# Optimization experiments

Measured on AMD Instinct MI355X. Metric: run time of the kernel, lower is better.

Reference implementation:

```python
import jax, jax.numpy as jnp
import numpy as np

N = 50000
E = 1600000
F_IN = 128
F_OUT = 64
NEG_SLOPE = 0.2


def setup_inputs() -> dict:
    key = jax.random.key(0)
    k1, k2, k3, k4, k5, k6 = jax.random.split(key, 6)
    x = jax.random.normal(k1, (N, F_IN), dtype=jnp.float32)
    edge_index = jax.random.randint(k2, (2, E), 0, N, dtype=jnp.int64)
    # GATConv params (heads=1): glorot-ish scale
    W = jax.random.normal(k3, (F_IN, F_OUT), dtype=jnp.float32) * (1.0 / np.sqrt(F_IN))
    att_src = jax.random.normal(k4, (F_OUT,), dtype=jnp.float32) * (1.0 / np.sqrt(F_OUT))
    att_dst = jax.random.normal(k5, (F_OUT,), dtype=jnp.float32) * (1.0 / np.sqrt(F_OUT))
    bias = jnp.zeros((F_OUT,), dtype=jnp.float32)
    return {"x": x, "edge_index": edge_index, "W": W, "att_src": att_src, "att_dst": att_dst, "bias": bias}


def _gat_forward(x, edge_index, W, att_src, att_dst, bias):
    n = x.shape[0]
    # add self loops (PyG GATConv default)
    loops = jnp.arange(n, dtype=edge_index.dtype)
    src = jnp.concatenate([edge_index[0], loops])  # [E+N]
    dst = jnp.concatenate([edge_index[1], loops])  # [E+N]

    h = x @ W                                      # [N, F_OUT]
    a_src = h @ att_src                            # [N]
    a_dst = h @ att_dst                            # [N]

    e = a_src[src] + a_dst[dst]                    # [E+N]
    e = jnp.where(e > 0, e, NEG_SLOPE * e)         # LeakyReLU(0.2)

    # softmax over edges grouped by destination node
    e_max = jax.ops.segment_max(e, dst, num_segments=n)     # [N]
    e_exp = jnp.exp(e - e_max[dst])                          # [E+N]
    e_sum = jax.ops.segment_sum(e_exp, dst, num_segments=n)  # [N]
    alpha = e_exp / e_sum[dst]                               # [E+N]

    msg = h[src] * alpha[:, None]                            # [E+N, F_OUT]
    out = jax.ops.segment_sum(msg, dst, num_segments=n)      # [N, F_OUT]
    out = out + bias
    return jax.nn.relu(out)


def reference(x, edge_index, W, att_src, att_dst, bias):
    return _gat_forward(x, edge_index, W, att_src, att_dst, bias)
```

## Files before the change

kernel.cpp:

```cpp
#include <hip/hip_runtime.h>

#define NN 50000
#define NE 1600000
#define FIN 128
#define FOUT 64
#define SLOPE 0.2f

#define NBC  63
#define NPC  800
#define CAPC 27500
#define NPB  16
#define NFPB 50
#define NBF  (NBC * NFPB)
#define CAPB 768
#define FBLK 261
#define CHC4 1536
#define GBLK 782
#define K2PB 8
#define LW   136

typedef unsigned int u32;
typedef short short8 __attribute__((ext_vector_type(8)));
typedef float f32x4 __attribute__((ext_vector_type(4)));

__device__ __forceinline__ unsigned short f2bf(float f) {
    u32 u = __float_as_uint(f);
    u += 0x7FFFu + ((u >> 16) & 1u);
    return (unsigned short)(u >> 16);
}
__device__ __forceinline__ float bf2f(unsigned short s) {
    return __uint_as_float(((u32)s) << 16);
}

union FusedLds {
    unsigned short Wt[64 * LW];
    struct { int cnt[4][64]; int gb[64]; int cur[64]; } f;
};

__global__ __launch_bounds__(256) void fused_k(
        const float* __restrict__ x, const float* __restrict__ W,
        const float* __restrict__ att_s, const float* __restrict__ att_d,
        const int* __restrict__ ei, int* __restrict__ ccur,
        u32* __restrict__ cstage, unsigned short* __restrict__ h,
        float* __restrict__ a_src, float* __restrict__ a_dst) {
    __shared__ FusedLds L;
    const int tid = threadIdx.x;

    if (blockIdx.x < FBLK) {
        const int wv = tid >> 6;
        ((int*)L.f.cnt)[tid] = 0;
        __syncthreads();
        const int4* sd4 = (const int4*)(ei + NE);
        const int4* ss4 = (const int4*)ei;
        const int lo = blockIdx.x * CHC4, hi = min(NE / 4, lo + CHC4);
        for (int i = lo + tid; i < hi; i += 256) {
            int4 d = sd4[i];
            atomicAdd(&L.f.cnt[wv][d.x / NPC], 1);
            atomicAdd(&L.f.cnt[wv][d.y / NPC], 1);
            atomicAdd(&L.f.cnt[wv][d.z / NPC], 1);
            atomicAdd(&L.f.cnt[wv][d.w / NPC], 1);
        }
        __syncthreads();
        if (tid < NBC) {
            int tot = L.f.cnt[0][tid] + L.f.cnt[1][tid]
                    + L.f.cnt[2][tid] + L.f.cnt[3][tid];
            L.f.gb[tid] = tot ? atomicAdd(&ccur[tid], tot) : 0;
            L.f.cur[tid] = 0;
        }
        __syncthreads();
        for (int i = lo + tid; i < hi; i += 256) {
            int4 d = sd4[i];
            int4 s = ss4[i];
            int b, pos;
            b = d.x / NPC; pos = L.f.gb[b] + atomicAdd(&L.f.cur[b], 1);
            if (pos < CAPC) cstage[b * CAPC + pos] = (u32)s.x | ((u32)(d.x - b * NPC) << 16);
            b = d.y / NPC; pos = L.f.gb[b] + atomicAdd(&L.f.cur[b], 1);
            if (pos < CAPC) cstage[b * CAPC + pos] = (u32)s.y | ((u32)(d.y - b * NPC) << 16);
            b = d.z / NPC; pos = L.f.gb[b] + atomicAdd(&L.f.cur[b], 1);
            if (pos < CAPC) cstage[b * CAPC + pos] = (u32)s.z | ((u32)(d.z - b * NPC) << 16);
            b = d.w / NPC; pos = L.f.gb[b] + atomicAdd(&L.f.cur[b], 1);
            if (pos < CAPC) cstage[b * CAPC + pos] = (u32)s.w | ((u32)(d.w - b * NPC) << 16);
        }
    } else {
        unsigned short* Wt = L.Wt;
        const int node0 = (blockIdx.x - FBLK) * 64;
        for (int i = tid; i < 128 * 16; i += 256) {
            int k = i >> 4, f = (i & 15) * 4;
            float4 w4 = ((const float4*)W)[i];
            Wt[(f + 0) * LW + k] = f2bf(w4.x);
            Wt[(f + 1) * LW + k] = f2bf(w4.y);
            Wt[(f + 2) * LW + k] = f2bf(w4.z);
            Wt[(f + 3) * LW + k] = f2bf(w4.w);
        }
        const int wv = tid >> 6, lane = tid & 63;
        const int q = lane >> 4, mr = lane & 15;
        const int row = node0 + wv * 16 + mr;
        const bool valid = row < NN;
        const float4* x4 = (const float4*)x;

        short8 afr[4];
        #pragma unroll
        for (int ks = 0; ks < 4; ++ks) {
            float4 f0 = make_float4(0.f, 0.f, 0.f, 0.f), f1 = f0;
            if (valid) {
                f0 = x4[(size_t)row * 32 + ks * 8 + q * 2];
                f1 = x4[(size_t)row * 32 + ks * 8 + q * 2 + 1];
            }
            short8 a;
            a[0] = (short)f2bf(f0.x); a[1] = (short)f2bf(f0.y);
            a[2] = (short)f2bf(f0.z); a[3] = (short)f2bf(f0.w);
            a[4] = (short)f2bf(f1.x); a[5] = (short)f2bf(f1.y);
            a[6] = (short)f2bf(f1.z); a[7] = (short)f2bf(f1.w);
            afr[ks] = a;
        }
        __syncthreads();

        f32x4 acc[4] = {{0,0,0,0},{0,0,0,0},{0,0,0,0},{0,0,0,0}};
        #pragma unroll
        for (int ks = 0; ks < 4; ++ks) {
            #pragma unroll
            for (int nt = 0; nt < 4; ++nt) {
                short8 b = *(const short8*)(Wt + (nt * 16 + mr) * LW + ks * 32 + q * 8);
                acc[nt] = __builtin_amdgcn_mfma_f32_16x16x32_bf16(afr[ks], b, acc[nt], 0, 0, 0);
            }
        }
        float atts[4], attd[4];
        #pragma unroll
        for (int nt = 0; nt < 4; ++nt) {
            atts[nt] = att_s[nt * 16 + mr];
            attd[nt] = att_d[nt * 16 + mr];
        }
        #pragma unroll
        for (int r = 0; r < 4; ++r) {
            int node = node0 + wv * 16 + q * 4 + r;
            float ps = 0.f, pd = 0.f;
            #pragma unroll
            for (int nt = 0; nt < 4; ++nt) {
                float v = acc[nt][r];
                if (node < NN) h[(size_t)node * 64 + nt * 16 + mr] = f2bf(v);
                ps += v * atts[nt];
                pd += v * attd[nt];
            }
            #pragma unroll
            for (int off = 8; off > 0; off >>= 1) {
                ps += __shfl_xor(ps, off);
                pd += __shfl_xor(pd, off);
            }
            if (mr == 0 && node < NN) { a_src[node] = ps; a_dst[node] = pd; }
        }
    }
}

__global__ __launch_bounds__(256) void fine_k(
        const u32* __restrict__ cstage, const int* __restrict__ ccur,
        int* __restrict__ fcur, u32* __restrict__ fstage) {
    const int bin = blockIdx.x / K2PB, sub = blockIdx.x % K2PB;
    const int size = min(ccur[bin], CAPC);
    const int qs = (size + K2PB - 1) / K2PB;
    const int lo = sub * qs, hi = min(size, lo + qs);
    const u32* src = cstage + (size_t)bin * CAPC;
    const int tid = threadIdx.x, wv = tid >> 6;

    __shared__ int cnt[4][64];
    __shared__ int gb[64];
    __shared__ int cur[64];
    ((int*)cnt)[tid] = 0;
    __syncthreads();
    for (int i = lo + tid; i < hi; i += 256)
        atomicAdd(&cnt[wv][(src[i] >> 16) >> 4], 1);
    __syncthreads();
    if (tid < NFPB) {
        int tot = cnt[0][tid] + cnt[1][tid] + cnt[2][tid] + cnt[3][tid];
        gb[tid] = tot ? atomicAdd(&fcur[bin * NFPB + tid], tot) : 0;
        cur[tid] = 0;
    }
    __syncthreads();
    for (int i = lo + tid; i < hi; i += 256) {
        u32 w = src[i];
        int dl = w >> 16;
        int f = dl >> 4;
        int pos = gb[f] + atomicAdd(&cur[f], 1);
        if (pos < CAPB)
            fstage[(size_t)(bin * NFPB + f) * CAPB + pos] =
                (w & 0xFFFFu) | ((u32)(dl & 15) << 16);
    }
}

__global__ __launch_bounds__(256) void agg_k(
        const u32* __restrict__ staging, const int* __restrict__ bcur,
        const float* __restrict__ a_src, const float* __restrict__ a_dst,
        const ushort4* __restrict__ h4, const float* __restrict__ bias,
        float* __restrict__ out) {
    const int bkt = blockIdx.x;
    const int node0 = bkt << 4;
    if (node0 >= NN) return;
    const int nNodes = min(NPB, NN - node0);
    const int bsize = min(bcur[bkt], CAPB);
    const u32* stg = staging + (size_t)bkt * CAPB;
    const int tid = threadIdx.x, wv = tid >> 6, lane = tid & 63;

    __shared__ u32 pk[CAPB];
    __shared__ unsigned short ssrc[CAPB];
    __shared__ int lcnt[NPB];
    __shared__ int lbase[NPB + 1];
    __shared__ int lcur[NPB];
    float* evals = (float*)pk;

    for (int j = tid; j < bsize; j += 256) pk[j] = stg[j];
    if (tid < NPB) lcnt[tid] = 0;
    __syncthreads();
    for (int j = tid; j < bsize; j += 256)
        atomicAdd(&lcnt[pk[j] >> 16], 1);
    __syncthreads();
    if (tid < 64) {
        int v = (tid < NPB) ? lcnt[tid] : 0;
        #pragma unroll
        for (int off = 1; off < NPB; off <<= 1) {
            int u = __shfl_up(v, off);
            if (tid >= off) v += u;
        }
        if (tid < NPB) lbase[tid + 1] = v;
        if (tid == 0) lbase[0] = 0;
    }
    if (tid >= 64 && tid < 64 + NPB) lcur[tid - 64] = 0;
    __syncthreads();
    for (int j = tid; j < bsize; j += 256) {
        u32 w = pk[j];
        int ld = w >> 16;
        int pos = lbase[ld] + atomicAdd(&lcur[ld], 1);
        ssrc[pos] = (unsigned short)(w & 0xFFFFu);
    }
    __syncthreads();

    const int q = lane >> 4, ql = lane & 15;
    const float4 b4 = ((const float4*)bias)[ql];
    const int ln = wv * 4 + q;
    if (ln >= nNodes) return;
    const int n = node0 + ln;
    const int st = lbase[ln], deg = lbase[ln + 1] - st;
    const float ad = a_dst[n];
    float es = a_src[n] + ad; es = es > 0.f ? es : SLOPE * es;
    const float ps = __expf(es);
    float sum = 0.f;
    for (int j = ql; j < deg; j += 16) {
        int s = ssrc[st + j];
        float e = a_src[s] + ad; e = e > 0.f ? e : SLOPE * e;
        float pe = __expf(e);
        evals[st + j] = pe;
        sum += pe;
    }
    sum += __shfl_xor(sum, 8); sum += __shfl_xor(sum, 4);
    sum += __shfl_xor(sum, 2); sum += __shfl_xor(sum, 1);
    const float inv = 1.f / (sum + ps);

    ushort4 hs = h4[(size_t)n * 16 + ql];
    float a0 = ps * bf2f(hs.x), a1 = ps * bf2f(hs.y);
    float a2 = ps * bf2f(hs.z), a3 = ps * bf2f(hs.w);
    int j = 0;
    for (; j + 4 <= deg; j += 4) {
        int s0 = ssrc[st + j], s1 = ssrc[st + j + 1];
        int s2 = ssrc[st + j + 2], s3 = ssrc[st + j + 3];
        float e0 = evals[st + j], e1 = evals[st + j + 1];
        float e2 = evals[st + j + 2], e3 = evals[st + j + 3];
        ushort4 v0 = h4[(size_t)s0 * 16 + ql];
        ushort4 v1 = h4[(size_t)s1 * 16 + ql];
        ushort4 v2 = h4[(size_t)s2 * 16 + ql];
        ushort4 v3 = h4[(size_t)s3 * 16 + ql];
        a0 += e0 * bf2f(v0.x); a1 += e0 * bf2f(v0.y);
        a2 += e0 * bf2f(v0.z); a3 += e0 * bf2f(v0.w);
        a0 += e1 * bf2f(v1.x); a1 += e1 * bf2f(v1.y);
        a2 += e1 * bf2f(v1.z); a3 += e1 * bf2f(v1.w);
        a0 += e2 * bf2f(v2.x); a1 += e2 * bf2f(v2.y);
        a2 += e2 * bf2f(v2.z); a3 += e2 * bf2f(v2.w);
        a0 += e3 * bf2f(v3.x); a1 += e3 * bf2f(v3.y);
        a2 += e3 * bf2f(v3.z); a3 += e3 * bf2f(v3.w);
    }
    for (; j < deg; ++j) {
        int s = ssrc[st + j];
        float ev = evals[st + j];
        ushort4 hv = h4[(size_t)s * 16 + ql];
        a0 += ev * bf2f(hv.x); a1 += ev * bf2f(hv.y);
        a2 += ev * bf2f(hv.z); a3 += ev * bf2f(hv.w);
    }
    float4 o;
    o.x = a0 * inv + b4.x; o.x = o.x > 0.f ? o.x : 0.f;
    o.y = a1 * inv + b4.y; o.y = o.y > 0.f ? o.y : 0.f;
    o.z = a2 * inv + b4.z; o.z = o.z > 0.f ? o.z : 0.f;
    o.w = a3 * inv + b4.w; o.w = o.w > 0.f ? o.w : 0.f;
    ((float4*)out)[(size_t)n * 16 + ql] = o;
}

extern "C" void kernel_launch(void* const* d_in, const int* in_sizes, int n_in,
                              void* d_out, int out_size, void* d_ws, size_t ws_size,
                              hipStream_t stream) {
    const float* x     = (const float*)d_in[0];
    const int*   ei    = (const int*)d_in[1];
    const float* W     = (const float*)d_in[2];
    const float* att_s = (const float*)d_in[3];
    const float* att_d = (const float*)d_in[4];
    const float* bias  = (const float*)d_in[5];
    float* out = (float*)d_out;

    unsigned short* h = (unsigned short*)d_ws;
    float* a_src  = (float*)(h + (size_t)NN * 64);
    float* a_dst  = a_src + NN;
    int*   ccur   = (int*)(a_dst + NN);
    int*   fcur   = ccur + 64;
    u32*   cstage = (u32*)(fcur + 3200);
    u32*   fstage = cstage + (size_t)NBC * CAPC;

    hipMemsetAsync(ccur, 0, (64 + 3200) * sizeof(int), stream);

    fused_k<<<FBLK + GBLK, 256, 0, stream>>>(x, W, att_s, att_d, ei, ccur,
                                             cstage, h, a_src, a_dst);
    fine_k<<<NBC * K2PB, 256, 0, stream>>>(cstage, ccur, fcur, fstage);
    agg_k<<<NBF, 256, 0, stream>>>(fstage, fcur, a_src, a_dst,
                                   (const ushort4*)h, bias, out);
}
```

Baseline: 143.4 us.

## Replace two-level edge binning with single-pass 64-node buckets

Drops the coarse/fine two-pass radix binning: the fused kernel now scatters edges directly into 782 buckets of 64 destination nodes each, and the separate fine_k kernel is removed. The aggregation kernel handles 64 nodes per block, with each 16-lane quad looping over 4 nodes. This saves one kernel launch and a full read/write pass over the staged edges. The cost is more global atomics per block (up to 782 bins), LDS counters spread across many bins, and fewer, larger aggregation blocks with serialized per-quad work.

```diff
diff --git a/kernel.cpp b/kernel.cpp
--- a/kernel.cpp
+++ b/kernel.cpp
@@ -6,17 +6,12 @@
 #define FOUT 64
 #define SLOPE 0.2f
 
-#define NBC  63
-#define NPC  800
-#define CAPC 27500
-#define NPB  16
-#define NFPB 50
-#define NBF  (NBC * NFPB)
-#define CAPB 768
+#define NPB  64
+#define NB   782
+#define CAP  2560
 #define FBLK 261
 #define CHC4 1536
 #define GBLK 782
-#define K2PB 8
 #define LW   136
 
 typedef unsigned int u32;
@@ -34,7 +29,7 @@
 
 union FusedLds {
     unsigned short Wt[64 * LW];
-    struct { int cnt[4][64]; int gb[64]; int cur[64]; } f;
+    struct { int cnt[NB]; int gb[NB]; int cur[NB]; } f;
 };
 
 __global__ __launch_bounds__(256) void fused_k(
@@ -47,39 +42,37 @@
     const int tid = threadIdx.x;
 
     if (blockIdx.x < FBLK) {
-        const int wv = tid >> 6;
-        ((int*)L.f.cnt)[tid] = 0;
+        for (int i = tid; i < NB; i += 256) L.f.cnt[i] = 0;
         __syncthreads();
         const int4* sd4 = (const int4*)(ei + NE);
         const int4* ss4 = (const int4*)ei;
         const int lo = blockIdx.x * CHC4, hi = min(NE / 4, lo + CHC4);
         for (int i = lo + tid; i < hi; i += 256) {
             int4 d = sd4[i];
-            atomicAdd(&L.f.cnt[wv][d.x / NPC], 1);
-            atomicAdd(&L.f.cnt[wv][d.y / NPC], 1);
-            atomicAdd(&L.f.cnt[wv][d.z / NPC], 1);
-            atomicAdd(&L.f.cnt[wv][d.w / NPC], 1);
-        }
-        __syncthreads();
-        if (tid < NBC) {
-            int tot = L.f.cnt[0][tid] + L.f.cnt[1][tid]
-                    + L.f.cnt[2][tid] + L.f.cnt[3][tid];
-            L.f.gb[tid] = tot ? atomicAdd(&ccur[tid], tot) : 0;
-            L.f.cur[tid] = 0;
+            atomicAdd(&L.f.cnt[d.x >> 6], 1);
+            atomicAdd(&L.f.cnt[d.y >> 6], 1);
+            atomicAdd(&L.f.cnt[d.z >> 6], 1);
+            atomicAdd(&L.f.cnt[d.w >> 6], 1);
+        }
+        __syncthreads();
+        for (int b = tid; b < NB; b += 256) {
+            int tot = L.f.cnt[b];
+            L.f.gb[b] = tot ? atomicAdd(&ccur[b], tot) : 0;
+            L.f.cur[b] = 0;
         }
         __syncthreads();
         for (int i = lo + tid; i < hi; i += 256) {
             int4 d = sd4[i];
             int4 s = ss4[i];
             int b, pos;
-            b = d.x / NPC; pos = L.f.gb[b] + atomicAdd(&L.f.cur[b], 1);
-            if (pos < CAPC) cstage[b * CAPC + pos] = (u32)s.x | ((u32)(d.x - b * NPC) << 16);
-            b = d.y / NPC; pos = L.f.gb[b] + atomicAdd(&L.f.cur[b], 1);
-            if (pos < CAPC) cstage[b * CAPC + pos] = (u32)s.y | ((u32)(d.y - b * NPC) << 16);
-            b = d.z / NPC; pos = L.f.gb[b] + atomicAdd(&L.f.cur[b], 1);
-            if (pos < CAPC) cstage[b * CAPC + pos] = (u32)s.z | ((u32)(d.z - b * NPC) << 16);
-            b = d.w / NPC; pos = L.f.gb[b] + atomicAdd(&L.f.cur[b], 1);
-            if (pos < CAPC) cstage[b * CAPC + pos] = (u32)s.w | ((u32)(d.w - b * NPC) << 16);
+            b = d.x >> 6; pos = L.f.gb[b] + atomicAdd(&L.f.cur[b], 1);
+            if (pos < CAP) cstage[(size_t)b * CAP + pos] = (u32)s.x | ((u32)(d.x & 63) << 16);
+            b = d.y >> 6; pos = L.f.gb[b] + atomicAdd(&L.f.cur[b], 1);
+            if (pos < CAP) cstage[(size_t)b * CAP + pos] = (u32)s.y | ((u32)(d.y & 63) << 16);
+            b = d.z >> 6; pos = L.f.gb[b] + atomicAdd(&L.f.cur[b], 1);
+            if (pos < CAP) cstage[(size_t)b * CAP + pos] = (u32)s.z | ((u32)(d.z & 63) << 16);
+            b = d.w >> 6; pos = L.f.gb[b] + atomicAdd(&L.f.cur[b], 1);
+            if (pos < CAP) cstage[(size_t)b * CAP + pos] = (u32)s.w | ((u32)(d.w & 63) << 16);
         }
     } else {
         unsigned short* Wt = L.Wt;
@@ -151,56 +144,20 @@
     }
 }
 
-__global__ __launch_bounds__(256) void fine_k(
-        const u32* __restrict__ cstage, const int* __restrict__ ccur,
-        int* __restrict__ fcur, u32* __restrict__ fstage) {
-    const int bin = blockIdx.x / K2PB, sub = blockIdx.x % K2PB;
-    const int size = min(ccur[bin], CAPC);
-    const int qs = (size + K2PB - 1) / K2PB;
-    const int lo = sub * qs, hi = min(size, lo + qs);
-    const u32* src = cstage + (size_t)bin * CAPC;
-    const int tid = threadIdx.x, wv = tid >> 6;
-
-    __shared__ int cnt[4][64];
-    __shared__ int gb[64];
-    __shared__ int cur[64];
-    ((int*)cnt)[tid] = 0;
-    __syncthreads();
-    for (int i = lo + tid; i < hi; i += 256)
-        atomicAdd(&cnt[wv][(src[i] >> 16) >> 4], 1);
-    __syncthreads();
-    if (tid < NFPB) {
-        int tot = cnt[0][tid] + cnt[1][tid] + cnt[2][tid] + cnt[3][tid];
-        gb[tid] = tot ? atomicAdd(&fcur[bin * NFPB + tid], tot) : 0;
-        cur[tid] = 0;
-    }
-    __syncthreads();
-    for (int i = lo + tid; i < hi; i += 256) {
-        u32 w = src[i];
-        int dl = w >> 16;
-        int f = dl >> 4;
-        int pos = gb[f] + atomicAdd(&cur[f], 1);
-        if (pos < CAPB)
-            fstage[(size_t)(bin * NFPB + f) * CAPB + pos] =
-                (w & 0xFFFFu) | ((u32)(dl & 15) << 16);
-    }
-}
-
 __global__ __launch_bounds__(256) void agg_k(
         const u32* __restrict__ staging, const int* __restrict__ bcur,
         const float* __restrict__ a_src, const float* __restrict__ a_dst,
         const ushort4* __restrict__ h4, const float* __restrict__ bias,
         float* __restrict__ out) {
     const int bkt = blockIdx.x;
-    const int node0 = bkt << 4;
-    if (node0 >= NN) return;
+    const int node0 = bkt << 6;
     const int nNodes = min(NPB, NN - node0);
-    const int bsize = min(bcur[bkt], CAPB);
-    const u32* stg = staging + (size_t)bkt * CAPB;
+    const int bsize = min(bcur[bkt], CAP);
+    const u32* stg = staging + (size_t)bkt * CAP;
     const int tid = threadIdx.x, wv = tid >> 6, lane = tid & 63;
 
-    __shared__ u32 pk[CAPB];
-    __shared__ unsigned short ssrc[CAPB];
+    __shared__ u32 pk[CAP];
+    __shared__ unsigned short ssrc[CAP];
     __shared__ int lcnt[NPB];
     __shared__ int lbase[NPB + 1];
     __shared__ int lcur[NPB];
@@ -213,13 +170,13 @@
         atomicAdd(&lcnt[pk[j] >> 16], 1);
     __syncthreads();
     if (tid < 64) {
-        int v = (tid < NPB) ? lcnt[tid] : 0;
-        #pragma unroll
-        for (int off = 1; off < NPB; off <<= 1) {
+        int v = lcnt[tid];
+        #pragma unroll
+        for (int off = 1; off < 64; off <<= 1) {
             int u = __shfl_up(v, off);
             if (tid >= off) v += u;
         }
-        if (tid < NPB) lbase[tid + 1] = v;
+        lbase[tid + 1] = v;
         if (tid == 0) lbase[0] = 0;
     }
     if (tid >= 64 && tid < 64 + NPB) lcur[tid - 64] = 0;
@@ -234,60 +191,63 @@
 
     const int q = lane >> 4, ql = lane & 15;
     const float4 b4 = ((const float4*)bias)[ql];
-    const int ln = wv * 4 + q;
-    if (ln >= nNodes) return;
-    const int n = node0 + ln;
-    const int st = lbase[ln], deg = lbase[ln + 1] - st;
-    const float ad = a_dst[n];
-    float es = a_src[n] + ad; es = es > 0.f ? es : SLOPE * es;
-    const float ps = __expf(es);
-    float sum = 0.f;
-    for (int j = ql; j < deg; j += 16) {
-        int s = ssrc[st + j];
-        float e = a_src[s] + ad; e = e > 0.f ? e : SLOPE * e;
-        float pe = __expf(e);
-        evals[st + j] = pe;
-        sum += pe;
-    }
-    sum += __shfl_xor(sum, 8); sum += __shfl_xor(sum, 4);
-    sum += __shfl_xor(sum, 2); sum += __shfl_xor(sum, 1);
-    const float inv = 1.f / (sum + ps);
-
-    ushort4 hs = h4[(size_t)n * 16 + ql];
-    float a0 = ps * bf2f(hs.x), a1 = ps * bf2f(hs.y);
-    float a2 = ps * bf2f(hs.z), a3 = ps * bf2f(hs.w);
-    int j = 0;
-    for (; j + 4 <= deg; j += 4) {
-        int s0 = ssrc[st + j], s1 = ssrc[st + j + 1];
-        int s2 = ssrc[st + j + 2], s3 = ssrc[st + j + 3];
-        float e0 = evals[st + j], e1 = evals[st + j + 1];
-        float e2 = evals[st + j + 2], e3 = evals[st + j + 3];
-        ushort4 v0 = h4[(size_t)s0 * 16 + ql];
-        ushort4 v1 = h4[(size_t)s1 * 16 + ql];
-        ushort4 v2 = h4[(size_t)s2 * 16 + ql];
-        ushort4 v3 = h4[(size_t)s3 * 16 + ql];
-        a0 += e0 * bf2f(v0.x); a1 += e0 * bf2f(v0.y);
-        a2 += e0 * bf2f(v0.z); a3 += e0 * bf2f(v0.w);
-        a0 += e1 * bf2f(v1.x); a1 += e1 * bf2f(v1.y);
-        a2 += e1 * bf2f(v1.z); a3 += e1 * bf2f(v1.w);
-        a0 += e2 * bf2f(v2.x); a1 += e2 * bf2f(v2.y);
-        a2 += e2 * bf2f(v2.z); a3 += e2 * bf2f(v2.w);
-        a0 += e3 * bf2f(v3.x); a1 += e3 * bf2f(v3.y);
-        a2 += e3 * bf2f(v3.z); a3 += e3 * bf2f(v3.w);
-    }
-    for (; j < deg; ++j) {
-        int s = ssrc[st + j];
-        float ev = evals[st + j];
-        ushort4 hv = h4[(size_t)s * 16 + ql];
-        a0 += ev * bf2f(hv.x); a1 += ev * bf2f(hv.y);
-        a2 += ev * bf2f(hv.z); a3 += ev * bf2f(hv.w);
-    }
-    float4 o;
-    o.x = a0 * inv + b4.x; o.x = o.x > 0.f ? o.x : 0.f;
-    o.y = a1 * inv + b4.y; o.y = o.y > 0.f ? o.y : 0.f;
-    o.z = a2 * inv + b4.z; o.z = o.z > 0.f ? o.z : 0.f;
-    o.w = a3 * inv + b4.w; o.w = o.w > 0.f ? o.w : 0.f;
-    ((float4*)out)[(size_t)n * 16 + ql] = o;
+    const int quad = wv * 4 + q;
+    for (int t = 0; t < 4; ++t) {
+        const int ln = quad * 4 + t;
+        if (ln >= nNodes) continue;
+        const int n = node0 + ln;
+        const int st = lbase[ln], deg = lbase[ln + 1] - st;
+        const float ad = a_dst[n];
+        float es = a_src[n] + ad; es = es > 0.f ? es : SLOPE * es;
+        const float ps = __expf(es);
+        float sum = 0.f;
+        for (int j = ql; j < deg; j += 16) {
+            int s = ssrc[st + j];
+            float e = a_src[s] + ad; e = e > 0.f ? e : SLOPE * e;
+            float pe = __expf(e);
+            evals[st + j] = pe;
+            sum += pe;
+        }
+        sum += __shfl_xor(sum, 8); sum += __shfl_xor(sum, 4);
+        sum += __shfl_xor(sum, 2); sum += __shfl_xor(sum, 1);
+        const float inv = 1.f / (sum + ps);
+
+        ushort4 hs = h4[(size_t)n * 16 + ql];
+        float a0 = ps * bf2f(hs.x), a1 = ps * bf2f(hs.y);
+        float a2 = ps * bf2f(hs.z), a3 = ps * bf2f(hs.w);
+        int j = 0;
+        for (; j + 4 <= deg; j += 4) {
+            int s0 = ssrc[st + j], s1 = ssrc[st + j + 1];
+            int s2 = ssrc[st + j + 2], s3 = ssrc[st + j + 3];
+            float e0 = evals[st + j], e1 = evals[st + j + 1];
+            float e2 = evals[st + j + 2], e3 = evals[st + j + 3];
+            ushort4 v0 = h4[(size_t)s0 * 16 + ql];
+            ushort4 v1 = h4[(size_t)s1 * 16 + ql];
+            ushort4 v2 = h4[(size_t)s2 * 16 + ql];
+            ushort4 v3 = h4[(size_t)s3 * 16 + ql];
+            a0 += e0 * bf2f(v0.x); a1 += e0 * bf2f(v0.y);
+            a2 += e0 * bf2f(v0.z); a3 += e0 * bf2f(v0.w);
+            a0 += e1 * bf2f(v1.x); a1 += e1 * bf2f(v1.y);
+            a2 += e1 * bf2f(v1.z); a3 += e1 * bf2f(v1.w);
+            a0 += e2 * bf2f(v2.x); a1 += e2 * bf2f(v2.y);
+            a2 += e2 * bf2f(v2.z); a3 += e2 * bf2f(v2.w);
+            a0 += e3 * bf2f(v3.x); a1 += e3 * bf2f(v3.y);
+            a2 += e3 * bf2f(v3.z); a3 += e3 * bf2f(v3.w);
+        }
+        for (; j < deg; ++j) {
+            int s = ssrc[st + j];
+            float ev = evals[st + j];
+            ushort4 hv = h4[(size_t)s * 16 + ql];
+            a0 += ev * bf2f(hv.x); a1 += ev * bf2f(hv.y);
+            a2 += ev * bf2f(hv.z); a3 += ev * bf2f(hv.w);
+        }
+        float4 o;
+        o.x = a0 * inv + b4.x; o.x = o.x > 0.f ? o.x : 0.f;
+        o.y = a1 * inv + b4.y; o.y = o.y > 0.f ? o.y : 0.f;
+        o.z = a2 * inv + b4.z; o.z = o.z > 0.f ? o.z : 0.f;
+        o.w = a3 * inv + b4.w; o.w = o.w > 0.f ? o.w : 0.f;
+        ((float4*)out)[(size_t)n * 16 + ql] = o;
+    }
 }
 
 extern "C" void kernel_launch(void* const* d_in, const int* in_sizes, int n_in,
@@ -305,15 +265,12 @@
     float* a_src  = (float*)(h + (size_t)NN * 64);
     float* a_dst  = a_src + NN;
     int*   ccur   = (int*)(a_dst + NN);
-    int*   fcur   = ccur + 64;
-    u32*   cstage = (u32*)(fcur + 3200);
-    u32*   fstage = cstage + (size_t)NBC * CAPC;
-
-    hipMemsetAsync(ccur, 0, (64 + 3200) * sizeof(int), stream);
+    u32*   cstage = (u32*)(ccur + 1024);
+
+    hipMemsetAsync(ccur, 0, NB * sizeof(int), stream);
 
     fused_k<<<FBLK + GBLK, 256, 0, stream>>>(x, W, att_s, att_d, ei, ccur,
                                              cstage, h, a_src, a_dst);
-    fine_k<<<NBC * K2PB, 256, 0, stream>>>(cstage, ccur, fcur, fstage);
-    agg_k<<<NBF, 256, 0, stream>>>(fstage, fcur, a_src, a_dst,
-                                   (const ushort4*)h, bias, out);
-}
+    agg_k<<<NB, 256, 0, stream>>>(cstage, ccur, a_src, a_dst,
+                                  (const ushort4*)h, bias, out);
+}
```

Measured after the change: 149.9 us. +4.5%, slower.

## Merge edge binning into GEMM blocks and cache edge data in registers

Applied to the files above, without the earlier changes.

Before, the fused kernel used separate block ranges, one for coarse edge binning and one for the x@W GEMM. Now every block first does its GEMM tile and then bins a 512-int4 chunk of edges (782*512 covers all 400000). Each edge is kept in registers between the count pass and the scatter pass, so the global index arrays are read once instead of twice. The fine pass is also split into 16 sub-blocks per bin instead of 8. The cost is a longer per-block critical path and extra syncthreads, and the GEMM and binning work no longer run in separate blocks side by side.

```diff
diff --git a/kernel.cpp b/kernel.cpp
--- a/kernel.cpp
+++ b/kernel.cpp
@@ -2,6 +2,7 @@
 
 #define NN 50000
 #define NE 1600000
+#define NE4 400000
 #define FIN 128
 #define FOUT 64
 #define SLOPE 0.2f
@@ -13,10 +14,9 @@
 #define NFPB 50
 #define NBF  (NBC * NFPB)
 #define CAPB 768
-#define FBLK 261
-#define CHC4 1536
 #define GBLK 782
-#define K2PB 8
+#define CHC4 512
+#define K2PB 16
 #define LW   136
 
 typedef unsigned int u32;
@@ -45,45 +45,11 @@
         float* __restrict__ a_src, float* __restrict__ a_dst) {
     __shared__ FusedLds L;
     const int tid = threadIdx.x;
-
-    if (blockIdx.x < FBLK) {
-        const int wv = tid >> 6;
-        ((int*)L.f.cnt)[tid] = 0;
-        __syncthreads();
-        const int4* sd4 = (const int4*)(ei + NE);
-        const int4* ss4 = (const int4*)ei;
-        const int lo = blockIdx.x * CHC4, hi = min(NE / 4, lo + CHC4);
-        for (int i = lo + tid; i < hi; i += 256) {
-            int4 d = sd4[i];
-            atomicAdd(&L.f.cnt[wv][d.x / NPC], 1);
-            atomicAdd(&L.f.cnt[wv][d.y / NPC], 1);
-            atomicAdd(&L.f.cnt[wv][d.z / NPC], 1);
-            atomicAdd(&L.f.cnt[wv][d.w / NPC], 1);
-        }
-        __syncthreads();
-        if (tid < NBC) {
-            int tot = L.f.cnt[0][tid] + L.f.cnt[1][tid]
-                    + L.f.cnt[2][tid] + L.f.cnt[3][tid];
-            L.f.gb[tid] = tot ? atomicAdd(&ccur[tid], tot) : 0;
-            L.f.cur[tid] = 0;
-        }
-        __syncthreads();
-        for (int i = lo + tid; i < hi; i += 256) {
-            int4 d = sd4[i];
-            int4 s = ss4[i];
-            int b, pos;
-            b = d.x / NPC; pos = L.f.gb[b] + atomicAdd(&L.f.cur[b], 1);
-            if (pos < CAPC) cstage[b * CAPC + pos] = (u32)s.x | ((u32)(d.x - b * NPC) << 16);
-            b = d.y / NPC; pos = L.f.gb[b] + atomicAdd(&L.f.cur[b], 1);
-            if (pos < CAPC) cstage[b * CAPC + pos] = (u32)s.y | ((u32)(d.y - b * NPC) << 16);
-            b = d.z / NPC; pos = L.f.gb[b] + atomicAdd(&L.f.cur[b], 1);
-            if (pos < CAPC) cstage[b * CAPC + pos] = (u32)s.z | ((u32)(d.z - b * NPC) << 16);
-            b = d.w / NPC; pos = L.f.gb[b] + atomicAdd(&L.f.cur[b], 1);
-            if (pos < CAPC) cstage[b * CAPC + pos] = (u32)s.w | ((u32)(d.w - b * NPC) << 16);
-        }
-    } else {
+    const int wv = tid >> 6, lane = tid & 63;
+
+    {
         unsigned short* Wt = L.Wt;
-        const int node0 = (blockIdx.x - FBLK) * 64;
+        const int node0 = blockIdx.x * 64;
         for (int i = tid; i < 128 * 16; i += 256) {
             int k = i >> 4, f = (i & 15) * 4;
             float4 w4 = ((const float4*)W)[i];
@@ -92,7 +58,6 @@
             Wt[(f + 2) * LW + k] = f2bf(w4.z);
             Wt[(f + 3) * LW + k] = f2bf(w4.w);
         }
-        const int wv = tid >> 6, lane = tid & 63;
         const int q = lane >> 4, mr = lane & 15;
         const int row = node0 + wv * 16 + mr;
         const bool valid = row < NN;
@@ -147,6 +112,53 @@
                 pd += __shfl_xor(pd, off);
             }
             if (mr == 0 && node < NN) { a_src[node] = ps; a_dst[node] = pd; }
+        }
+    }
+    __syncthreads();
+
+    ((int*)L.f.cnt)[tid] = 0;
+    __syncthreads();
+
+    const int4* sd4 = (const int4*)(ei + NE);
+    const int4* ss4 = (const int4*)ei;
+    const int lo = blockIdx.x * CHC4;
+    int bkx[2][4];
+    u32 payx[2][4];
+    #pragma unroll
+    for (int u = 0; u < 2; ++u) {
+        const int i = lo + tid + u * 256;
+        if (i < NE4) {
+            int4 d = sd4[i];
+            int4 s = ss4[i];
+            bkx[u][0] = d.x / NPC; payx[u][0] = (u32)s.x | ((u32)(d.x - bkx[u][0] * NPC) << 16);
+            bkx[u][1] = d.y / NPC; payx[u][1] = (u32)s.y | ((u32)(d.y - bkx[u][1] * NPC) << 16);
+            bkx[u][2] = d.z / NPC; payx[u][2] = (u32)s.z | ((u32)(d.z - bkx[u][2] * NPC) << 16);
+            bkx[u][3] = d.w / NPC; payx[u][3] = (u32)s.w | ((u32)(d.w - bkx[u][3] * NPC) << 16);
+            atomicAdd(&L.f.cnt[wv][bkx[u][0]], 1);
+            atomicAdd(&L.f.cnt[wv][bkx[u][1]], 1);
+            atomicAdd(&L.f.cnt[wv][bkx[u][2]], 1);
+            atomicAdd(&L.f.cnt[wv][bkx[u][3]], 1);
+        } else {
+            bkx[u][0] = bkx[u][1] = bkx[u][2] = bkx[u][3] = -1;
+        }
+    }
+    __syncthreads();
+    if (tid < NBC) {
+        int tot = L.f.cnt[0][tid] + L.f.cnt[1][tid]
+                + L.f.cnt[2][tid] + L.f.cnt[3][tid];
+        L.f.gb[tid] = tot ? atomicAdd(&ccur[tid], tot) : 0;
+        L.f.cur[tid] = 0;
+    }
+    __syncthreads();
+    #pragma unroll
+    for (int u = 0; u < 2; ++u) {
+        #pragma unroll
+        for (int e = 0; e < 4; ++e) {
+            int b = bkx[u][e];
+            if (b >= 0) {
+                int pos = L.f.gb[b] + atomicAdd(&L.f.cur[b], 1);
+                if (pos < CAPC) cstage[(size_t)b * CAPC + pos] = payx[u][e];
+            }
         }
     }
 }
@@ -311,8 +323,8 @@
 
     hipMemsetAsync(ccur, 0, (64 + 3200) * sizeof(int), stream);
 
-    fused_k<<<FBLK + GBLK, 256, 0, stream>>>(x, W, att_s, att_d, ei, ccur,
-                                             cstage, h, a_src, a_dst);
+    fused_k<<<GBLK, 256, 0, stream>>>(x, W, att_s, att_d, ei, ccur,
+                                      cstage, h, a_src, a_dst);
     fine_k<<<NBC * K2PB, 256, 0, stream>>>(cstage, ccur, fcur, fstage);
     agg_k<<<NBF, 256, 0, stream>>>(fstage, fcur, a_src, a_dst,
                                    (const ushort4*)h, bias, out);
```

Result: no change. 144.0 us (+0.4%).
